# Kernel tuning notes

Hardware: AMD Instinct MI355X
Metric: run time of the kernel (lower is better)

The kernel has to match this reference:

```python
import jax, jax.numpy as jnp
import numpy as np

N, IN_F, OUT_F = 1024, 256, 1024

def setup_inputs() -> dict:
    key = jax.random.key(0)
    k1, k2 = jax.random.split(key)
    x = jax.random.normal(k1, (N, IN_F), dtype=jnp.float32)
    centres = jax.random.normal(k2, (OUT_F, IN_F), dtype=jnp.float32)  # normal_(0,1) init
    log_sigmas = jnp.zeros((OUT_F,), dtype=jnp.float32)  # constant_(0) init
    return {"x": x, "centres": centres, "log_sigmas": log_sigmas}

def reference(x, centres, log_sigmas):
    # diff: (N, out_features, in_features) broadcast, matching torch expand
    diff = x[:, None, :] - centres[None, :, :]
    # Euclidean distance then per-centre sigma scaling: (N, out_features)
    distances = jnp.sqrt(jnp.sum(diff * diff, axis=-1)) / jnp.exp(log_sigmas)[None, :]
    # gaussian basis function: exp(-0.5 * d^2)
    return jnp.exp(-0.5 * distances * distances)
```

## Files before the change

kernel.cpp:

```cpp
#include <hip/hip_runtime.h>
#include <math.h>

#define K_FEAT 256
#define M_OUT  1024
#define N_ROWS 1024

#define TM 64
#define TN 32
#define LSTR 264

typedef short bf16x8 __attribute__((ext_vector_type(8)));
typedef float f32x4  __attribute__((ext_vector_type(4)));

__global__ __launch_bounds__(256, 2) void rbf_mfma(
    const float* __restrict__ x,
    const float* __restrict__ centres,
    const float* __restrict__ log_sigmas,
    float* __restrict__ out)
{
    __shared__ unsigned short xs[TM * LSTR];
    __shared__ unsigned short cs[TN * LSTR];
    __shared__ float nx[TM];
    __shared__ float nc[TN];

    const int tid  = threadIdx.x;
    const int lane = tid & 63;
    const int wave = tid >> 6;
    const int row_base = blockIdx.y * TM;
    const int col_base = blockIdx.x * TN;

    #pragma unroll
    for (int l = 0; l < 12; ++l) {
        const int  li    = (l < 8) ? l : (l - 8);
        const int  chunk = tid + li * 256;
        const int  row   = chunk >> 5;
        const int  k0    = (chunk & 31) * 8;
        const float* src = (l < 8)
            ? (x       + (size_t)(row_base + row) * K_FEAT + k0)
            : (centres + (size_t)(col_base + row) * K_FEAT + k0);
        const float4 v0 = ((const float4*)src)[0];
        const float4 v1 = ((const float4*)src)[1];
        uint4 p;
        p.x = (__float_as_uint(v0.x) >> 16) | (__float_as_uint(v0.y) & 0xffff0000u);
        p.y = (__float_as_uint(v0.z) >> 16) | (__float_as_uint(v0.w) & 0xffff0000u);
        p.z = (__float_as_uint(v1.x) >> 16) | (__float_as_uint(v1.y) & 0xffff0000u);
        p.w = (__float_as_uint(v1.z) >> 16) | (__float_as_uint(v1.w) & 0xffff0000u);
        unsigned short* dst = (l < 8) ? &xs[row * LSTR + k0] : &cs[row * LSTR + k0];
        *(uint4*)dst = p;
    }
    __syncthreads();

    if (tid < TM + TN) {
        const unsigned short* src = (tid < TM) ? &xs[tid * LSTR] : &cs[(tid - TM) * LSTR];
        float s0 = 0.f, s1 = 0.f, s2 = 0.f, s3 = 0.f;
        #pragma unroll
        for (int k = 0; k < K_FEAT; k += 8) {
            const uint4 q = *(const uint4*)(src + k);
            const float f0 = __uint_as_float(q.x << 16);
            const float f1 = __uint_as_float(q.x & 0xffff0000u);
            const float f2 = __uint_as_float(q.y << 16);
            const float f3 = __uint_as_float(q.y & 0xffff0000u);
            const float f4 = __uint_as_float(q.z << 16);
            const float f5 = __uint_as_float(q.z & 0xffff0000u);
            const float f6 = __uint_as_float(q.w << 16);
            const float f7 = __uint_as_float(q.w & 0xffff0000u);
            s0 = fmaf(f0, f0, s0); s1 = fmaf(f1, f1, s1);
            s2 = fmaf(f2, f2, s2); s3 = fmaf(f3, f3, s3);
            s0 = fmaf(f4, f4, s0); s1 = fmaf(f5, f5, s1);
            s2 = fmaf(f6, f6, s2); s3 = fmaf(f7, f7, s3);
        }
        const float s = (s0 + s1) + (s2 + s3);
        if (tid < TM) nx[tid] = s; else nc[tid - TM] = s;
    }

    const int m    = lane & 15;
    const int quad = lane >> 4;
    const int row_slab = wave * 16;
    f32x4 acc0 = {0.f, 0.f, 0.f, 0.f};
    f32x4 acc1 = {0.f, 0.f, 0.f, 0.f};
    const unsigned short* ap  = &xs[(row_slab + m) * LSTR + quad * 8];
    const unsigned short* bp0 = &cs[ m       * LSTR + quad * 8];
    const unsigned short* bp1 = &cs[(16 + m) * LSTR + quad * 8];
    #pragma unroll
    for (int kk = 0; kk < 8; ++kk) {
        const bf16x8 a  = *(const bf16x8*)(ap  + kk * 32);
        const bf16x8 b0 = *(const bf16x8*)(bp0 + kk * 32);
        const bf16x8 b1 = *(const bf16x8*)(bp1 + kk * 32);
        acc0 = __builtin_amdgcn_mfma_f32_16x16x32_bf16(a, b0, acc0, 0, 0, 0);
        acc1 = __builtin_amdgcn_mfma_f32_16x16x32_bf16(a, b1, acc1, 0, 0, 0);
    }
    __syncthreads();

    const int col0 = col_base + m;
    const int col1 = col_base + 16 + m;
    const float i2s0 = __expf(-2.0f * log_sigmas[col0]);
    const float i2s1 = __expf(-2.0f * log_sigmas[col1]);
    const float ncv0 = nc[m];
    const float ncv1 = nc[16 + m];
    #pragma unroll
    for (int i = 0; i < 4; ++i) {
        const int r = row_slab + quad * 4 + i;
        const float nxv = nx[r];
        const float d0 = nxv + ncv0 - 2.0f * acc0[i];
        const float d1 = nxv + ncv1 - 2.0f * acc1[i];
        float* o = out + (size_t)(row_base + r) * M_OUT;
        o[col0] = __expf(-0.5f * d0 * i2s0);
        o[col1] = __expf(-0.5f * d1 * i2s1);
    }
}

extern "C" void kernel_launch(void* const* d_in, const int* in_sizes, int n_in,
                              void* d_out, int out_size, void* d_ws, size_t ws_size,
                              hipStream_t stream) {
    const float* x  = (const float*)d_in[0];
    const float* c  = (const float*)d_in[1];
    const float* ls = (const float*)d_in[2];
    float* out = (float*)d_out;

    dim3 grid(M_OUT / TN, N_ROWS / TM);
    rbf_mfma<<<grid, dim3(256), 0, stream>>>(x, c, ls, out);
}
```

Measured before the change: 62.12 us.

## Precompute bf16 operands and norms in a prep kernel; load tiles directly into LDS

Adds a prep kernel that converts x and centres to bf16 once, stores them in workspace with an XOR-swizzled layout, and computes the row norms and inverse sigma squared. The main kernel then copies its tiles into LDS with global_load_lds, with no register round trip. Tiles shrink to 32x32 so each of the four waves computes one 16x16 MFMA block. This removes the repeated per-tile fp32-to-bf16 conversion and norm computation, and halves global read bytes in the main kernel. In exchange it adds a second kernel launch and a workspace round trip.

```diff
diff --git a/kernel.cpp b/kernel.cpp
--- a/kernel.cpp
+++ b/kernel.cpp
@@ -1,111 +1,130 @@
 #include <hip/hip_runtime.h>
 #include <math.h>
+
 
 #define K_FEAT 256
 #define M_OUT  1024
 #define N_ROWS 1024
 
-#define TM 64
+#define TM 32
 #define TN 32
-#define LSTR 264
 
 typedef short bf16x8 __attribute__((ext_vector_type(8)));
 typedef float f32x4  __attribute__((ext_vector_type(4)));
 
-__global__ __launch_bounds__(256, 2) void rbf_mfma(
+
+__device__ __forceinline__ void gl_lds16(const unsigned short* g, unsigned short* l)
+{
+    __builtin_amdgcn_global_load_lds(
+        (const __attribute__((address_space(1))) void*)(unsigned long long)g,
+        (__attribute__((address_space(3))) void*)(unsigned int)(unsigned long long)l,
+        16, 0, 0);
+}
+
+__global__ __launch_bounds__(256) void rbf_prep(
     const float* __restrict__ x,
     const float* __restrict__ centres,
     const float* __restrict__ log_sigmas,
+    unsigned short* __restrict__ xb,
+    unsigned short* __restrict__ cb,
+    float* __restrict__ nx,
+    float* __restrict__ nc,
+    float* __restrict__ sc)
+{
+    const int tid  = threadIdx.x;
+    const int lane = tid & 63;
+    const int wave = tid >> 6;
+    const int g    = blockIdx.x * 4 + wave;
+    const bool isx = (g < N_ROWS);
+    const int  r   = isx ? g : (g - N_ROWS);
+
+    const float* src = (isx ? x : centres) + (size_t)r * K_FEAT;
+    const float4 v = ((const float4*)src)[lane];
+
+    const unsigned int ux = __float_as_uint(v.x);
+    const unsigned int uy = __float_as_uint(v.y);
+    const unsigned int uz = __float_as_uint(v.z);
+    const unsigned int uw = __float_as_uint(v.w);
+
+    uint2 pk;
+    pk.x = (ux >> 16) | (uy & 0xffff0000u);
+    pk.y = (uz >> 16) | (uw & 0xffff0000u);
+
+    const float f0 = __uint_as_float(ux & 0xffff0000u);
+    const float f1 = __uint_as_float(uy & 0xffff0000u);
+    const float f2 = __uint_as_float(uz & 0xffff0000u);
+    const float f3 = __uint_as_float(uw & 0xffff0000u);
+    float s = fmaf(f0, f0, fmaf(f1, f1, fmaf(f2, f2, f3 * f3)));
+    #pragma unroll
+    for (int off = 32; off; off >>= 1) s += __shfl_xor(s, off, 64);
+
+    const int idx = (lane * 4) ^ ((r & 7) << 3);
+    unsigned short* dst = (isx ? xb : cb) + (size_t)r * K_FEAT + idx;
+    *(uint2*)dst = pk;
+
+    if (lane == 0) (isx ? nx : nc)[r] = s;
+
+    if (blockIdx.x < 4) {
+        const int t = blockIdx.x * 256 + tid;
+        sc[t] = __expf(-2.0f * log_sigmas[t]);
+    }
+}
+
+__global__ __launch_bounds__(256, 4) void rbf_main(
+    const unsigned short* __restrict__ xb,
+    const unsigned short* __restrict__ cb,
+    const float* __restrict__ nx,
+    const float* __restrict__ nc,
+    const float* __restrict__ sc,
     float* __restrict__ out)
 {
-    __shared__ unsigned short xs[TM * LSTR];
-    __shared__ unsigned short cs[TN * LSTR];
-    __shared__ float nx[TM];
-    __shared__ float nc[TN];
+    __shared__ unsigned short xs[TM * K_FEAT];
+    __shared__ unsigned short cs[TN * K_FEAT];
 
     const int tid  = threadIdx.x;
     const int lane = tid & 63;
     const int wave = tid >> 6;
+    const int m    = lane & 15;
+    const int quad = lane >> 4;
+    const int wr   = wave >> 1;
+    const int wc   = wave & 1;
     const int row_base = blockIdx.y * TM;
     const int col_base = blockIdx.x * TN;
 
+    const unsigned short* xg = xb + (size_t)row_base * K_FEAT;
+    const unsigned short* cg = cb + (size_t)col_base * K_FEAT;
     #pragma unroll
-    for (int l = 0; l < 12; ++l) {
-        const int  li    = (l < 8) ? l : (l - 8);
-        const int  chunk = tid + li * 256;
-        const int  row   = chunk >> 5;
-        const int  k0    = (chunk & 31) * 8;
-        const float* src = (l < 8)
-            ? (x       + (size_t)(row_base + row) * K_FEAT + k0)
-            : (centres + (size_t)(col_base + row) * K_FEAT + k0);
-        const float4 v0 = ((const float4*)src)[0];
-        const float4 v1 = ((const float4*)src)[1];
-        uint4 p;
-        p.x = (__float_as_uint(v0.x) >> 16) | (__float_as_uint(v0.y) & 0xffff0000u);
-        p.y = (__float_as_uint(v0.z) >> 16) | (__float_as_uint(v0.w) & 0xffff0000u);
-        p.z = (__float_as_uint(v1.x) >> 16) | (__float_as_uint(v1.y) & 0xffff0000u);
-        p.w = (__float_as_uint(v1.z) >> 16) | (__float_as_uint(v1.w) & 0xffff0000u);
-        unsigned short* dst = (l < 8) ? &xs[row * LSTR + k0] : &cs[row * LSTR + k0];
-        *(uint4*)dst = p;
-    }
+    for (int j = 0; j < 4; ++j)
+        gl_lds16(xg + j * 2048 + tid * 8, xs + j * 2048 + tid * 8);
+    #pragma unroll
+    for (int j = 0; j < 4; ++j)
+        gl_lds16(cg + j * 2048 + tid * 8, cs + j * 2048 + tid * 8);
     __syncthreads();
 
-    if (tid < TM + TN) {
-        const unsigned short* src = (tid < TM) ? &xs[tid * LSTR] : &cs[(tid - TM) * LSTR];
-        float s0 = 0.f, s1 = 0.f, s2 = 0.f, s3 = 0.f;
-        #pragma unroll
-        for (int k = 0; k < K_FEAT; k += 8) {
-            const uint4 q = *(const uint4*)(src + k);
-            const float f0 = __uint_as_float(q.x << 16);
-            const float f1 = __uint_as_float(q.x & 0xffff0000u);
-            const float f2 = __uint_as_float(q.y << 16);
-            const float f3 = __uint_as_float(q.y & 0xffff0000u);
-            const float f4 = __uint_as_float(q.z << 16);
-            const float f5 = __uint_as_float(q.z & 0xffff0000u);
-            const float f6 = __uint_as_float(q.w << 16);
-            const float f7 = __uint_as_float(q.w & 0xffff0000u);
-            s0 = fmaf(f0, f0, s0); s1 = fmaf(f1, f1, s1);
-            s2 = fmaf(f2, f2, s2); s3 = fmaf(f3, f3, s3);
-            s0 = fmaf(f4, f4, s0); s1 = fmaf(f5, f5, s1);
-            s2 = fmaf(f6, f6, s2); s3 = fmaf(f7, f7, s3);
-        }
-        const float s = (s0 + s1) + (s2 + s3);
-        if (tid < TM) nx[tid] = s; else nc[tid - TM] = s;
+    const int ar = wr * 16 + m;
+    const int br = wc * 16 + m;
+    const int sA = (ar & 7) << 3;
+    const int sB = (br & 7) << 3;
+    const unsigned short* pa = xs + ar * K_FEAT;
+    const unsigned short* pb = cs + br * K_FEAT;
+
+    f32x4 acc = {0.f, 0.f, 0.f, 0.f};
+    #pragma unroll
+    for (int kk = 0; kk < 8; ++kk) {
+        const int k0 = quad * 8 + kk * 32;
+        const bf16x8 a = *(const bf16x8*)(pa + (k0 ^ sA));
+        const bf16x8 b = *(const bf16x8*)(pb + (k0 ^ sB));
+        acc = __builtin_amdgcn_mfma_f32_16x16x32_bf16(a, b, acc, 0, 0, 0);
     }
 
-    const int m    = lane & 15;
-    const int quad = lane >> 4;
-    const int row_slab = wave * 16;
-    f32x4 acc0 = {0.f, 0.f, 0.f, 0.f};
-    f32x4 acc1 = {0.f, 0.f, 0.f, 0.f};
-    const unsigned short* ap  = &xs[(row_slab + m) * LSTR + quad * 8];
-    const unsigned short* bp0 = &cs[ m       * LSTR + quad * 8];
-    const unsigned short* bp1 = &cs[(16 + m) * LSTR + quad * 8];
-    #pragma unroll
-    for (int kk = 0; kk < 8; ++kk) {
-        const bf16x8 a  = *(const bf16x8*)(ap  + kk * 32);
-        const bf16x8 b0 = *(const bf16x8*)(bp0 + kk * 32);
-        const bf16x8 b1 = *(const bf16x8*)(bp1 + kk * 32);
-        acc0 = __builtin_amdgcn_mfma_f32_16x16x32_bf16(a, b0, acc0, 0, 0, 0);
-        acc1 = __builtin_amdgcn_mfma_f32_16x16x32_bf16(a, b1, acc1, 0, 0, 0);
-    }
-    __syncthreads();
-
-    const int col0 = col_base + m;
-    const int col1 = col_base + 16 + m;
-    const float i2s0 = __expf(-2.0f * log_sigmas[col0]);
-    const float i2s1 = __expf(-2.0f * log_sigmas[col1]);
-    const float ncv0 = nc[m];
-    const float ncv1 = nc[16 + m];
+    const int   col = col_base + wc * 16 + m;
+    const float i2s = sc[col];
+    const float ncv = nc[col];
     #pragma unroll
     for (int i = 0; i < 4; ++i) {
-        const int r = row_slab + quad * 4 + i;
-        const float nxv = nx[r];
-        const float d0 = nxv + ncv0 - 2.0f * acc0[i];
-        const float d1 = nxv + ncv1 - 2.0f * acc1[i];
-        float* o = out + (size_t)(row_base + r) * M_OUT;
-        o[col0] = __expf(-0.5f * d0 * i2s0);
-        o[col1] = __expf(-0.5f * d1 * i2s1);
+        const int   gr = row_base + wr * 16 + quad * 4 + i;
+        const float d  = nx[gr] + ncv - 2.0f * acc[i];
+        out[(size_t)gr * M_OUT + col] = __expf(-0.5f * d * i2s);
     }
 }
 
@@ -117,6 +136,13 @@
     const float* ls = (const float*)d_in[2];
     float* out = (float*)d_out;
 
-    dim3 grid(M_OUT / TN, N_ROWS / TM);
-    rbf_mfma<<<grid, dim3(256), 0, stream>>>(x, c, ls, out);
+    unsigned short* xb = (unsigned short*)d_ws;
+    unsigned short* cb = xb + (size_t)N_ROWS * K_FEAT;
+    float* nx = (float*)((char*)d_ws + (1u << 20));
+    float* nc = nx + 1024;
+    float* sc = nc + 1024;
+
+    rbf_prep<<<dim3(512), dim3(256), 0, stream>>>(x, c, ls, xb, cb, nx, nc, sc);
+    rbf_main<<<dim3(M_OUT / TN, N_ROWS / TM), dim3(256), 0, stream>>>(
+        xb, cb, nx, nc, sc, out);
 }
```

Result: no change. 62.88 us (+1.2%).

## Fuse row-norm computation into load loop and swizzle LDS layout

Applied to the files above, without the earlier changes.

Computes the squared norms of the bf16-truncated rows while loading global data, using a wave shuffle reduction. This replaces the separate serial pass over shared memory done by only 96 threads. Shared memory padding is replaced by an XOR swizzle on the column offset, which cuts LDS size. The second barrier is removed and launch bounds ask for 3 blocks per CU. The trade-off is extra shuffle work and more register pressure in the load loop.

```diff
diff --git a/kernel.cpp b/kernel.cpp
--- a/kernel.cpp
+++ b/kernel.cpp
@@ -1,5 +1,6 @@
 #include <hip/hip_runtime.h>
 #include <math.h>
+
 
 #define K_FEAT 256
 #define M_OUT  1024
@@ -7,89 +8,90 @@
 
 #define TM 64
 #define TN 32
-#define LSTR 264
 
 typedef short bf16x8 __attribute__((ext_vector_type(8)));
 typedef float f32x4  __attribute__((ext_vector_type(4)));
 
-__global__ __launch_bounds__(256, 2) void rbf_mfma(
+__global__ __launch_bounds__(256, 3) void rbf_fused(
     const float* __restrict__ x,
     const float* __restrict__ centres,
     const float* __restrict__ log_sigmas,
     float* __restrict__ out)
 {
-    __shared__ unsigned short xs[TM * LSTR];
-    __shared__ unsigned short cs[TN * LSTR];
+    __shared__ unsigned short xs[TM * K_FEAT];
+    __shared__ unsigned short cs[TN * K_FEAT];
     __shared__ float nx[TM];
     __shared__ float nc[TN];
 
     const int tid  = threadIdx.x;
     const int lane = tid & 63;
-    const int wave = tid >> 6;
     const int row_base = blockIdx.y * TM;
     const int col_base = blockIdx.x * TN;
 
     #pragma unroll
-    for (int l = 0; l < 12; ++l) {
-        const int  li    = (l < 8) ? l : (l - 8);
-        const int  chunk = tid + li * 256;
-        const int  row   = chunk >> 5;
-        const int  k0    = (chunk & 31) * 8;
-        const float* src = (l < 8)
+    for (int li = 0; li < 12; ++li) {
+        const bool isx  = (li < 8);
+        const int chunk = tid + (isx ? li : li - 8) * 256;
+        const int row   = chunk >> 5;
+        const int k0    = (chunk & 31) * 8;
+        const float* src = isx
             ? (x       + (size_t)(row_base + row) * K_FEAT + k0)
             : (centres + (size_t)(col_base + row) * K_FEAT + k0);
         const float4 v0 = ((const float4*)src)[0];
         const float4 v1 = ((const float4*)src)[1];
+
+        const unsigned a0 = __float_as_uint(v0.x), a1 = __float_as_uint(v0.y);
+        const unsigned a2 = __float_as_uint(v0.z), a3 = __float_as_uint(v0.w);
+        const unsigned a4 = __float_as_uint(v1.x), a5 = __float_as_uint(v1.y);
+        const unsigned a6 = __float_as_uint(v1.z), a7 = __float_as_uint(v1.w);
+
         uint4 p;
-        p.x = (__float_as_uint(v0.x) >> 16) | (__float_as_uint(v0.y) & 0xffff0000u);
-        p.y = (__float_as_uint(v0.z) >> 16) | (__float_as_uint(v0.w) & 0xffff0000u);
-        p.z = (__float_as_uint(v1.x) >> 16) | (__float_as_uint(v1.y) & 0xffff0000u);
-        p.w = (__float_as_uint(v1.z) >> 16) | (__float_as_uint(v1.w) & 0xffff0000u);
-        unsigned short* dst = (l < 8) ? &xs[row * LSTR + k0] : &cs[row * LSTR + k0];
+        p.x = (a0 >> 16) | (a1 & 0xffff0000u);
+        p.y = (a2 >> 16) | (a3 & 0xffff0000u);
+        p.z = (a4 >> 16) | (a5 & 0xffff0000u);
+        p.w = (a6 >> 16) | (a7 & 0xffff0000u);
+
+        const float t0 = __uint_as_float(a0 & 0xffff0000u);
+        const float t1 = __uint_as_float(a1 & 0xffff0000u);
+        const float t2 = __uint_as_float(a2 & 0xffff0000u);
+        const float t3 = __uint_as_float(a3 & 0xffff0000u);
+        const float t4 = __uint_as_float(a4 & 0xffff0000u);
+        const float t5 = __uint_as_float(a5 & 0xffff0000u);
+        const float t6 = __uint_as_float(a6 & 0xffff0000u);
+        const float t7 = __uint_as_float(a7 & 0xffff0000u);
+        float s = fmaf(t0, t0, fmaf(t1, t1, fmaf(t2, t2, t3 * t3)))
+                + fmaf(t4, t4, fmaf(t5, t5, fmaf(t6, t6, t7 * t7)));
+        #pragma unroll
+        for (int off = 16; off; off >>= 1) s += __shfl_xor(s, off, 64);
+
+        unsigned short* dst = (isx ? xs : cs)
+                            + row * K_FEAT + (k0 ^ ((row & 7) << 3));
         *(uint4*)dst = p;
+        if ((tid & 31) == 0) (isx ? nx : nc)[row] = s;
     }
     __syncthreads();
 
-    if (tid < TM + TN) {
-        const unsigned short* src = (tid < TM) ? &xs[tid * LSTR] : &cs[(tid - TM) * LSTR];
-        float s0 = 0.f, s1 = 0.f, s2 = 0.f, s3 = 0.f;
-        #pragma unroll
-        for (int k = 0; k < K_FEAT; k += 8) {
-            const uint4 q = *(const uint4*)(src + k);
-            const float f0 = __uint_as_float(q.x << 16);
-            const float f1 = __uint_as_float(q.x & 0xffff0000u);
-            const float f2 = __uint_as_float(q.y << 16);
-            const float f3 = __uint_as_float(q.y & 0xffff0000u);
-            const float f4 = __uint_as_float(q.z << 16);
-            const float f5 = __uint_as_float(q.z & 0xffff0000u);
-            const float f6 = __uint_as_float(q.w << 16);
-            const float f7 = __uint_as_float(q.w & 0xffff0000u);
-            s0 = fmaf(f0, f0, s0); s1 = fmaf(f1, f1, s1);
-            s2 = fmaf(f2, f2, s2); s3 = fmaf(f3, f3, s3);
-            s0 = fmaf(f4, f4, s0); s1 = fmaf(f5, f5, s1);
-            s2 = fmaf(f6, f6, s2); s3 = fmaf(f7, f7, s3);
-        }
-        const float s = (s0 + s1) + (s2 + s3);
-        if (tid < TM) nx[tid] = s; else nc[tid - TM] = s;
-    }
-
+    const int wave = tid >> 6;
     const int m    = lane & 15;
     const int quad = lane >> 4;
-    const int row_slab = wave * 16;
+    const int ar   = wave * 16 + m;
+    const int sA   = (ar & 7) << 3;
+    const int sB   = (m & 7) << 3;
+    const unsigned short* pa  = xs + ar * K_FEAT;
+    const unsigned short* pb0 = cs +  m        * K_FEAT;
+    const unsigned short* pb1 = cs + (16 + m)  * K_FEAT;
+
     f32x4 acc0 = {0.f, 0.f, 0.f, 0.f};
     f32x4 acc1 = {0.f, 0.f, 0.f, 0.f};
-    const unsigned short* ap  = &xs[(row_slab + m) * LSTR + quad * 8];
-    const unsigned short* bp0 = &cs[ m       * LSTR + quad * 8];
-    const unsigned short* bp1 = &cs[(16 + m) * LSTR + quad * 8];
     #pragma unroll
     for (int kk = 0; kk < 8; ++kk) {
-        const bf16x8 a  = *(const bf16x8*)(ap  + kk * 32);
-        const bf16x8 b0 = *(const bf16x8*)(bp0 + kk * 32);
-        const bf16x8 b1 = *(const bf16x8*)(bp1 + kk * 32);
+        const int k0 = quad * 8 + kk * 32;
+        const bf16x8 a  = *(const bf16x8*)(pa  + (k0 ^ sA));
+        const bf16x8 b0 = *(const bf16x8*)(pb0 + (k0 ^ sB));
+        const bf16x8 b1 = *(const bf16x8*)(pb1 + (k0 ^ sB));
         acc0 = __builtin_amdgcn_mfma_f32_16x16x32_bf16(a, b0, acc0, 0, 0, 0);
         acc1 = __builtin_amdgcn_mfma_f32_16x16x32_bf16(a, b1, acc1, 0, 0, 0);
     }
-    __syncthreads();
 
     const int col0 = col_base + m;
     const int col1 = col_base + 16 + m;
@@ -99,7 +101,7 @@
     const float ncv1 = nc[16 + m];
     #pragma unroll
     for (int i = 0; i < 4; ++i) {
-        const int r = row_slab + quad * 4 + i;
+        const int r = wave * 16 + quad * 4 + i;
         const float nxv = nx[r];
         const float d0 = nxv + ncv0 - 2.0f * acc0[i];
         const float d1 = nxv + ncv1 - 2.0f * acc1[i];
@@ -118,5 +120,5 @@
     float* out = (float*)d_out;
 
     dim3 grid(M_OUT / TN, N_ROWS / TM);
-    rbf_mfma<<<grid, dim3(256), 0, stream>>>(x, c, ls, out);
+    rbf_fused<<<grid, dim3(256), 0, stream>>>(x, c, ls, out);
 }
```

Result: slower. 64.93 us (+4.5%).
